# Performance work log

Hardware: AMD Instinct MI355X
Metric: run time of the kernel (lower is better)

## Reference

```python
import jax, jax.numpy as jnp
import numpy as np

EPS = 1e-5
DN = ('NCDHW', 'OIDHW', 'NCDHW')

def conv3d(x, w, b):
    y = jax.lax.conv_general_dilated(x, w, (1, 1, 1), 'SAME', dimension_numbers=DN)
    return y + b[None, :, None, None, None]

def batchnorm(x, gamma, beta):
    # training-mode BatchNorm3d: biased batch stats over (N, D, H, W) per channel
    mean = jnp.mean(x, axis=(0, 2, 3, 4), keepdims=True)
    var = jnp.mean((x - mean) ** 2, axis=(0, 2, 3, 4), keepdims=True)
    xhat = (x - mean) * jax.lax.rsqrt(var + EPS)
    return gamma[None, :, None, None, None] * xhat + beta[None, :, None, None, None]

def setup_inputs() -> dict:
    key = jax.random.key(0)
    ks = jax.random.split(key, 8)
    C, N = 32, 4  # channel, fuzzynum
    B, D, H, W = 4, 64, 64, 64
    x = jax.random.normal(ks[0], (B, C, D, H, W), dtype=jnp.float32)
    fan1 = C * 27
    conv1_w = jax.random.uniform(ks[1], (1, C, 3, 3, 3), jnp.float32, -1, 1) / np.sqrt(fan1)
    conv1_b = jnp.zeros((1,), jnp.float32)
    fan2 = 1 * 27
    conv2_w = jax.random.uniform(ks[2], (C, 1, 3, 3, 3), jnp.float32, -1, 1) / np.sqrt(fan2)
    conv2_b = jnp.zeros((C,), jnp.float32)
    mu = jax.random.normal(ks[3], (C, N), dtype=jnp.float32)
    sigma = jax.random.normal(ks[4], (C, N), dtype=jnp.float32)
    bn1_g = jnp.ones((1,), jnp.float32)
    bn1_b = jnp.zeros((1,), jnp.float32)
    bn2_g = jnp.ones((C,), jnp.float32)
    bn2_b = jnp.zeros((C,), jnp.float32)
    return {"x": x, "conv1_w": conv1_w, "conv1_b": conv1_b, "conv2_w": conv2_w,
            "conv2_b": conv2_b, "mu": mu, "sigma": sigma,
            "bn1_g": bn1_g, "bn1_b": bn1_b, "bn2_g": bn2_g, "bn2_b": bn2_b}

def reference(x, conv1_w, conv1_b, conv2_w, conv2_b, mu, sigma, bn1_g, bn1_b, bn2_g, bn2_b):
    x1 = conv3d(x, conv1_w, conv1_b)                      # [B,1,D,H,W]
    # fuzzy Gaussian membership: only channel 0 of mu/sigma is used (x1 has 1 channel)
    m = mu[0]                                             # [n]
    s = sigma[0]                                          # [n]
    z = (x1[..., None] - m) / s                           # [B,1,D,H,W,n]
    fuzz = jnp.exp(-jnp.sum(z * z, axis=-1))              # [B,1,D,H,W]
    y = batchnorm(fuzz, bn1_g, bn1_b)
    y = conv3d(y, conv2_w, conv2_b)                       # [B,C,D,H,W]
    return batchnorm(y, bn2_g, bn2_b)
```

## Files before the change

kernel.cpp:

```cpp
#include <hip/hip_runtime.h>

constexpr int Cc = 32;
constexpr int SP = 64 * 64 * 64;
constexpr int TS = 4 * SP;


__global__ __launch_bounds__(256) void k_conv1_fuzzy(
    const float* __restrict__ x, const float* __restrict__ w1,
    const float* __restrict__ b1, const float* __restrict__ mu,
    const float* __restrict__ sg, float* __restrict__ fuzz,
    float* __restrict__ acc)
{
    const int tid = threadIdx.x;
    const int t = blockIdx.x * 256 + tid;
    const int wq = t & 15;        const int w0 = wq << 2;
    const int zp = (t >> 4) & 31; const int z0 = zp << 1;
    const int y  = (t >> 9) & 63;
    const int b  = t >> 15;
    const int lane = tid & 63;

    float S1 = 0.f, S2 = 0.f, S3 = 0.f;
#pragma unroll
    for (int n = 0; n < 4; n++) {
        float m = mu[n], s = sg[n];
        float iv = 1.0f / (s * s);
        S1 += iv; S2 += m * iv; S3 += m * m * iv;
    }

    const float b1v = b1[0];
    float a00 = b1v, a01 = b1v, a02 = b1v, a03 = b1v;
    float a10 = b1v, a11 = b1v, a12 = b1v, a13 = b1v;

    const float* xb = x + (size_t)b * Cc * SP;

    for (int c = 0; c < Cc; c++) {
        const float* xc = xb + c * SP;
        const float* wc = w1 + c * 27;

        float4 M[4][3];
#pragma unroll
        for (int rz = 0; rz < 4; rz++) {
            const int zz = z0 - 1 + rz;
            const bool okz = (unsigned)zz < 64u;
#pragma unroll
            for (int dy = 0; dy < 3; dy++) {
                const int yy = y - 1 + dy;
                float4 m = make_float4(0.f, 0.f, 0.f, 0.f);
                if (okz && (unsigned)yy < 64u)
                    m = *(const float4*)(xc + (zz << 12) + (yy << 6) + w0);
                M[rz][dy] = m;
            }
        }

        float L[4][3], R[4][3];
#pragma unroll
        for (int rz = 0; rz < 4; rz++)
#pragma unroll
            for (int dy = 0; dy < 3; dy++) {
                float lv = __shfl(M[rz][dy].w, (lane + 63) & 63, 64);
                float rv = __shfl(M[rz][dy].x, (lane + 1) & 63, 64);
                L[rz][dy] = (wq > 0)  ? lv : 0.f;
                R[rz][dy] = (wq < 15) ? rv : 0.f;
            }

#pragma unroll
        for (int rz = 0; rz < 4; rz++) {
#pragma unroll
            for (int dy = 0; dy < 3; dy++) {
                const float v0 = L[rz][dy];
                const float v1 = M[rz][dy].x, v2 = M[rz][dy].y;
                const float v3 = M[rz][dy].z, v4 = M[rz][dy].w;
                const float v5 = R[rz][dy];
                if (rz < 3) {
                    const float* wr = wc + (rz * 3 + dy) * 3;
                    const float W0 = wr[0], W1 = wr[1], W2 = wr[2];
                    a00 = fmaf(v0, W0, fmaf(v1, W1, fmaf(v2, W2, a00)));
                    a01 = fmaf(v1, W0, fmaf(v2, W1, fmaf(v3, W2, a01)));
                    a02 = fmaf(v2, W0, fmaf(v3, W1, fmaf(v4, W2, a02)));
                    a03 = fmaf(v3, W0, fmaf(v4, W1, fmaf(v5, W2, a03)));
                }
                if (rz >= 1) {
                    const float* wr = wc + ((rz - 1) * 3 + dy) * 3;
                    const float W0 = wr[0], W1 = wr[1], W2 = wr[2];
                    a10 = fmaf(v0, W0, fmaf(v1, W1, fmaf(v2, W2, a10)));
                    a11 = fmaf(v1, W0, fmaf(v2, W1, fmaf(v3, W2, a11)));
                    a12 = fmaf(v2, W0, fmaf(v3, W1, fmaf(v4, W2, a12)));
                    a13 = fmaf(v3, W0, fmaf(v4, W1, fmaf(v5, W2, a13)));
                }
            }
        }
    }

    float fsum = 0.f, fsq = 0.f;
#pragma unroll
    for (int oz = 0; oz < 2; oz++) {
        float xv[4] = { oz ? a10 : a00, oz ? a11 : a01,
                        oz ? a12 : a02, oz ? a13 : a03 };
        float4 fv;
        float* fp = &fv.x;
#pragma unroll
        for (int ow = 0; ow < 4; ow++) {
            float x1 = xv[ow];
            float tt = x1 * x1 * S1 - 2.0f * x1 * S2 + S3;
            float fz = __expf(-tt);
            fp[ow] = fz;
            fsum += fz; fsq += fz * fz;
        }
        *(float4*)(fuzz + (size_t)b * SP + ((z0 + oz) << 12) + (y << 6) + w0) = fv;
    }

#pragma unroll
    for (int m = 1; m < 64; m <<= 1) {
        fsum += __shfl_xor(fsum, m, 64);
        fsq  += __shfl_xor(fsq,  m, 64);
    }
    __shared__ float red[8];
    int wid = tid >> 6;
    if ((tid & 63) == 0) { red[wid * 2] = fsum; red[wid * 2 + 1] = fsq; }
    __syncthreads();
    if (tid == 0) {
        atomicAdd(&acc[0], red[0] + red[2] + red[4] + red[6]);
        atomicAdd(&acc[1], red[1] + red[3] + red[5] + red[7]);
    }
}

__global__ void k_fin1(const float* __restrict__ g, const float* __restrict__ be,
                       float* __restrict__ acc)
{
    float mean = acc[0] * (1.0f / TS);
    float var  = acc[1] * (1.0f / TS) - mean * mean;
    float a = g[0] * rsqrtf(var + 1e-5f);
    acc[2] = a;
    acc[3] = be[0] - mean * a;
}

__global__ __launch_bounds__(256) void k_conv2(
    const float* __restrict__ fuzz, const float* __restrict__ w2,
    const float* __restrict__ b2, const float* __restrict__ acc,
    float* __restrict__ out)
{
    const int p = blockIdx.x * 256 + threadIdx.x;
    const int w = p & 63, y = (p >> 6) & 63, z = (p >> 12) & 63, b = p >> 18;
    const float a = acc[2], sh = acc[3];
    const bool wl = (w > 0), wr = (w < 63);
    const float* fb = fuzz + (size_t)b * SP;

    float v[27];
#pragma unroll
    for (int dz = 0; dz < 3; dz++) {
        int zz = z + dz - 1;
        bool mz = (unsigned)zz < 64u;
#pragma unroll
        for (int dy = 0; dy < 3; dy++) {
            int yy = y + dy - 1;
            bool my = (unsigned)yy < 64u;
            int i = (dz * 3 + dy) * 3;
            float vl = 0.f, vm = 0.f, vr = 0.f;
            if (mz && my) {
                const float* row = fb + (zz << 12) + (yy << 6) + w;
                vm = fmaf(a, row[0], sh);
                if (wl) vl = fmaf(a, row[-1], sh);
                if (wr) vr = fmaf(a, row[1], sh);
            }
            v[i] = vl; v[i + 1] = vm; v[i + 2] = vr;
        }
    }

    float* ob = out + (size_t)b * Cc * SP + (p - b * SP);
#pragma unroll 4
    for (int c = 0; c < Cc; c++) {
        const float* wc = w2 + c * 27;
        float o = b2[c];
#pragma unroll
        for (int j = 0; j < 27; j++) o = fmaf(v[j], wc[j], o);
        ob[(size_t)c * SP] = o;
    }
}

__global__ __launch_bounds__(256) void k_stats2(const float4* __restrict__ out4,
                                                float* __restrict__ acc)
{
    int blk = blockIdx.x;
    int c = (blk >> 5) & 31;
    const float4* pp = out4 + (size_t)blk * 2048 + threadIdx.x;
    float s = 0.f, q = 0.f;
#pragma unroll
    for (int i = 0; i < 8; i++) {
        float4 v = pp[i * 256];
        s += v.x + v.y + v.z + v.w;
        q += v.x * v.x + v.y * v.y + v.z * v.z + v.w * v.w;
    }
#pragma unroll
    for (int m = 1; m < 64; m <<= 1) {
        s += __shfl_xor(s, m, 64);
        q += __shfl_xor(q, m, 64);
    }
    __shared__ float red[8];
    int lane = threadIdx.x & 63, wid = threadIdx.x >> 6;
    if (lane == 0) { red[wid * 2] = s; red[wid * 2 + 1] = q; }
    __syncthreads();
    if (threadIdx.x == 0) {
        atomicAdd(&acc[4 + c],  red[0] + red[2] + red[4] + red[6]);
        atomicAdd(&acc[36 + c], red[1] + red[3] + red[5] + red[7]);
    }
}

__global__ void k_fin2(const float* __restrict__ g, const float* __restrict__ be,
                       float* __restrict__ acc)
{
    int c = threadIdx.x;
    float mean = acc[4 + c] * (1.0f / TS);
    float var  = acc[36 + c] * (1.0f / TS) - mean * mean;
    float sc = g[c] * rsqrtf(var + 1e-5f);
    acc[68 + c]  = sc;
    acc[100 + c] = be[c] - mean * sc;
}

__global__ __launch_bounds__(256) void k_norm(float4* __restrict__ out4,
                                              const float* __restrict__ acc)
{
    size_t i = (size_t)blockIdx.x * 256 + threadIdx.x;
    int c = (int)((i >> 16) & 31);
    float sc = acc[68 + c], sh = acc[100 + c];
    float4 v = out4[i];
    v.x = fmaf(v.x, sc, sh);
    v.y = fmaf(v.y, sc, sh);
    v.z = fmaf(v.z, sc, sh);
    v.w = fmaf(v.w, sc, sh);
    out4[i] = v;
}

extern "C" void kernel_launch(void* const* d_in, const int* in_sizes, int n_in,
                              void* d_out, int out_size, void* d_ws, size_t ws_size,
                              hipStream_t stream)
{
    const float* x   = (const float*)d_in[0];
    const float* w1  = (const float*)d_in[1];
    const float* b1  = (const float*)d_in[2];
    const float* w2  = (const float*)d_in[3];
    const float* b2  = (const float*)d_in[4];
    const float* mu  = (const float*)d_in[5];
    const float* sg  = (const float*)d_in[6];
    const float* g1  = (const float*)d_in[7];
    const float* be1 = (const float*)d_in[8];
    const float* g2  = (const float*)d_in[9];
    const float* be2 = (const float*)d_in[10];

    float* out  = (float*)d_out;
    float* fuzz = (float*)d_ws;
    float* acc  = fuzz + TS;

    hipMemsetAsync(acc, 0, 132 * sizeof(float), stream);
    k_conv1_fuzzy<<<512, 256, 0, stream>>>(x, w1, b1, mu, sg, fuzz, acc);
    k_fin1<<<1, 1, 0, stream>>>(g1, be1, acc);
    k_conv2<<<TS / 256, 256, 0, stream>>>(fuzz, w2, b2, acc, out);
    k_stats2<<<4096, 256, 0, stream>>>((const float4*)out, acc);
    k_fin2<<<1, 32, 0, stream>>>(g2, be2, acc);
    k_norm<<<32768, 256, 0, stream>>>((float4*)out, acc);
}
```

Measured before the change: 439.9 us.

## Recompute conv2 for stats and fuse normalization into a single output write

Conv2 is now computed twice. The first pass produces only per-channel sums and sums of squares, reduced in shared memory and never written to memory. The second pass recomputes conv2 and writes the normalized output directly. This removes one full write and two full read/write passes over the 134 MB output tensor, at the cost of doubling the cheap conv2 arithmetic and the fuzz reads. It also register-blocks several z outputs per thread, shares neighbors across lanes with wave shuffles, and double-buffers the conv1 channel loads so the next channel's loads are issued before the current channel's compute.

```diff
diff --git a/kernel.cpp b/kernel.cpp
--- a/kernel.cpp
+++ b/kernel.cpp
@@ -33,55 +33,51 @@
 
     const float* xb = x + (size_t)b * Cc * SP;
 
-    for (int c = 0; c < Cc; c++) {
-        const float* xc = xb + c * SP;
+    bool pv[12]; int ofs[12];
+#pragma unroll
+    for (int rz = 0; rz < 4; rz++) {
+        const int zz = z0 - 1 + rz;
+        const bool okz = (unsigned)zz < 64u;
+#pragma unroll
+        for (int dy = 0; dy < 3; dy++) {
+            const int yy = y - 1 + dy;
+            pv[rz * 3 + dy]  = okz && ((unsigned)yy < 64u);
+            ofs[rz * 3 + dy] = (zz << 12) + (yy << 6) + w0;
+        }
+    }
+
+    auto LOADCH = [&](int c, float4 (&M)[12]) {
+        const float* xc = xb + (size_t)c * SP;
+#pragma unroll
+        for (int i = 0; i < 12; i++)
+            M[i] = pv[i] ? *(const float4*)(xc + ofs[i])
+                         : make_float4(0.f, 0.f, 0.f, 0.f);
+    };
+
+    auto COMPUTECH = [&](int c, const float4 (&M)[12]) {
         const float* wc = w1 + c * 27;
-
-        float4 M[4][3];
+        float Wv[27];
+#pragma unroll
+        for (int k = 0; k < 27; k++) Wv[k] = wc[k];
 #pragma unroll
         for (int rz = 0; rz < 4; rz++) {
-            const int zz = z0 - 1 + rz;
-            const bool okz = (unsigned)zz < 64u;
 #pragma unroll
             for (int dy = 0; dy < 3; dy++) {
-                const int yy = y - 1 + dy;
-                float4 m = make_float4(0.f, 0.f, 0.f, 0.f);
-                if (okz && (unsigned)yy < 64u)
-                    m = *(const float4*)(xc + (zz << 12) + (yy << 6) + w0);
-                M[rz][dy] = m;
-            }
-        }
-
-        float L[4][3], R[4][3];
-#pragma unroll
-        for (int rz = 0; rz < 4; rz++)
-#pragma unroll
-            for (int dy = 0; dy < 3; dy++) {
-                float lv = __shfl(M[rz][dy].w, (lane + 63) & 63, 64);
-                float rv = __shfl(M[rz][dy].x, (lane + 1) & 63, 64);
-                L[rz][dy] = (wq > 0)  ? lv : 0.f;
-                R[rz][dy] = (wq < 15) ? rv : 0.f;
-            }
-
-#pragma unroll
-        for (int rz = 0; rz < 4; rz++) {
-#pragma unroll
-            for (int dy = 0; dy < 3; dy++) {
-                const float v0 = L[rz][dy];
-                const float v1 = M[rz][dy].x, v2 = M[rz][dy].y;
-                const float v3 = M[rz][dy].z, v4 = M[rz][dy].w;
-                const float v5 = R[rz][dy];
+                const float4 m = M[rz * 3 + dy];
+                const float lv = __shfl(m.w, (lane + 63) & 63, 64);
+                const float rv = __shfl(m.x, (lane + 1) & 63, 64);
+                const float v0 = (wq > 0)  ? lv : 0.f;
+                const float v5 = (wq < 15) ? rv : 0.f;
+                const float v1 = m.x, v2 = m.y, v3 = m.z, v4 = m.w;
                 if (rz < 3) {
-                    const float* wr = wc + (rz * 3 + dy) * 3;
-                    const float W0 = wr[0], W1 = wr[1], W2 = wr[2];
+                    const float W0 = Wv[(rz*3+dy)*3], W1 = Wv[(rz*3+dy)*3+1], W2 = Wv[(rz*3+dy)*3+2];
                     a00 = fmaf(v0, W0, fmaf(v1, W1, fmaf(v2, W2, a00)));
                     a01 = fmaf(v1, W0, fmaf(v2, W1, fmaf(v3, W2, a01)));
                     a02 = fmaf(v2, W0, fmaf(v3, W1, fmaf(v4, W2, a02)));
                     a03 = fmaf(v3, W0, fmaf(v4, W1, fmaf(v5, W2, a03)));
                 }
                 if (rz >= 1) {
-                    const float* wr = wc + ((rz - 1) * 3 + dy) * 3;
-                    const float W0 = wr[0], W1 = wr[1], W2 = wr[2];
+                    const float W0 = Wv[((rz-1)*3+dy)*3], W1 = Wv[((rz-1)*3+dy)*3+1], W2 = Wv[((rz-1)*3+dy)*3+2];
                     a10 = fmaf(v0, W0, fmaf(v1, W1, fmaf(v2, W2, a10)));
                     a11 = fmaf(v1, W0, fmaf(v2, W1, fmaf(v3, W2, a11)));
                     a12 = fmaf(v2, W0, fmaf(v3, W1, fmaf(v4, W2, a12)));
@@ -89,6 +85,15 @@
                 }
             }
         }
+    };
+
+    float4 Ma[12], Mb[12];
+    LOADCH(0, Ma);
+    for (int c = 0; c < Cc; c += 2) {
+        LOADCH(c + 1, Mb);
+        COMPUTECH(c, Ma);
+        if (c + 2 < Cc) LOADCH(c + 2, Ma);
+        COMPUTECH(c + 1, Mb);
     }
 
     float fsum = 0.f, fsq = 0.f;
@@ -96,26 +101,23 @@
     for (int oz = 0; oz < 2; oz++) {
         float xv[4] = { oz ? a10 : a00, oz ? a11 : a01,
                         oz ? a12 : a02, oz ? a13 : a03 };
-        float4 fv;
-        float* fp = &fv.x;
+        float4 fv; float* fp = &fv.x;
 #pragma unroll
         for (int ow = 0; ow < 4; ow++) {
             float x1 = xv[ow];
             float tt = x1 * x1 * S1 - 2.0f * x1 * S2 + S3;
             float fz = __expf(-tt);
-            fp[ow] = fz;
-            fsum += fz; fsq += fz * fz;
+            fp[ow] = fz; fsum += fz; fsq += fz * fz;
         }
         *(float4*)(fuzz + (size_t)b * SP + ((z0 + oz) << 12) + (y << 6) + w0) = fv;
     }
-
 #pragma unroll
     for (int m = 1; m < 64; m <<= 1) {
         fsum += __shfl_xor(fsum, m, 64);
         fsq  += __shfl_xor(fsq,  m, 64);
     }
     __shared__ float red[8];
-    int wid = tid >> 6;
+    const int wid = tid >> 6;
     if ((tid & 63) == 0) { red[wid * 2] = fsum; red[wid * 2 + 1] = fsq; }
     __syncthreads();
     if (tid == 0) {
@@ -134,74 +136,81 @@
     acc[3] = be[0] - mean * a;
 }
 
-__global__ __launch_bounds__(256) void k_conv2(
+__global__ __launch_bounds__(256) void k_conv2_stats(
     const float* __restrict__ fuzz, const float* __restrict__ w2,
-    const float* __restrict__ b2, const float* __restrict__ acc,
-    float* __restrict__ out)
-{
-    const int p = blockIdx.x * 256 + threadIdx.x;
-    const int w = p & 63, y = (p >> 6) & 63, z = (p >> 12) & 63, b = p >> 18;
+    const float* __restrict__ b2, float* __restrict__ acc)
+{
+    const int tid = threadIdx.x;
+    const int t = blockIdx.x * 256 + tid;
+    const int lane = tid & 63;
+    const int w = t & 63;
+    const int y = (t >> 6) & 63;
+    const int z0 = ((t >> 12) & 15) << 2;
+    const int b = t >> 16;
     const float a = acc[2], sh = acc[3];
-    const bool wl = (w > 0), wr = (w < 63);
     const float* fb = fuzz + (size_t)b * SP;
 
-    float v[27];
-#pragma unroll
-    for (int dz = 0; dz < 3; dz++) {
-        int zz = z + dz - 1;
-        bool mz = (unsigned)zz < 64u;
+    float Fl[6][3], Fm[6][3], Fr[6][3];
+#pragma unroll
+    for (int rz = 0; rz < 6; rz++) {
+        const int zz = z0 - 1 + rz;
+        const bool okz = (unsigned)zz < 64u;
 #pragma unroll
         for (int dy = 0; dy < 3; dy++) {
-            int yy = y + dy - 1;
-            bool my = (unsigned)yy < 64u;
-            int i = (dz * 3 + dy) * 3;
-            float vl = 0.f, vm = 0.f, vr = 0.f;
-            if (mz && my) {
-                const float* row = fb + (zz << 12) + (yy << 6) + w;
-                vm = fmaf(a, row[0], sh);
-                if (wl) vl = fmaf(a, row[-1], sh);
-                if (wr) vr = fmaf(a, row[1], sh);
-            }
-            v[i] = vl; v[i + 1] = vm; v[i + 2] = vr;
-        }
-    }
-
-    float* ob = out + (size_t)b * Cc * SP + (p - b * SP);
-#pragma unroll 4
+            const int yy = y - 1 + dy;
+            float f = 0.f;
+            if (okz && (unsigned)yy < 64u)
+                f = fmaf(a, fb[(zz << 12) + (yy << 6) + w], sh);
+            const float lv = __shfl(f, (lane + 63) & 63, 64);
+            const float rv = __shfl(f, (lane + 1) & 63, 64);
+            Fm[rz][dy] = f;
+            Fl[rz][dy] = (w > 0)  ? lv : 0.f;
+            Fr[rz][dy] = (w < 63) ? rv : 0.f;
+        }
+    }
+
+    __shared__ float red[2][32][4];
+    const int wid = tid >> 6;
+
+#pragma unroll
     for (int c = 0; c < Cc; c++) {
         const float* wc = w2 + c * 27;
-        float o = b2[c];
-#pragma unroll
-        for (int j = 0; j < 27; j++) o = fmaf(v[j], wc[j], o);
-        ob[(size_t)c * SP] = o;
-    }
-}
-
-__global__ __launch_bounds__(256) void k_stats2(const float4* __restrict__ out4,
-                                                float* __restrict__ acc)
-{
-    int blk = blockIdx.x;
-    int c = (blk >> 5) & 31;
-    const float4* pp = out4 + (size_t)blk * 2048 + threadIdx.x;
-    float s = 0.f, q = 0.f;
-#pragma unroll
-    for (int i = 0; i < 8; i++) {
-        float4 v = pp[i * 256];
-        s += v.x + v.y + v.z + v.w;
-        q += v.x * v.x + v.y * v.y + v.z * v.z + v.w * v.w;
-    }
-#pragma unroll
-    for (int m = 1; m < 64; m <<= 1) {
-        s += __shfl_xor(s, m, 64);
-        q += __shfl_xor(q, m, 64);
-    }
-    __shared__ float red[8];
-    int lane = threadIdx.x & 63, wid = threadIdx.x >> 6;
-    if (lane == 0) { red[wid * 2] = s; red[wid * 2 + 1] = q; }
+        float Wv[27];
+#pragma unroll
+        for (int k = 0; k < 27; k++) Wv[k] = wc[k];
+        const float bb = b2[c];
+        float o0 = bb, o1 = bb, o2 = bb, o3 = bb;
+#pragma unroll
+        for (int rz = 0; rz < 6; rz++) {
+#pragma unroll
+            for (int dy = 0; dy < 3; dy++) {
+                const float l = Fl[rz][dy], m = Fm[rz][dy], r = Fr[rz][dy];
+#pragma unroll
+                for (int oz = 0; oz < 4; oz++) {
+                    const int dz = rz - oz;
+                    if (dz < 0 || dz > 2) continue;
+                    const float W0 = Wv[(dz*3+dy)*3], W1 = Wv[(dz*3+dy)*3+1], W2 = Wv[(dz*3+dy)*3+2];
+                    if      (oz == 0) o0 = fmaf(l, W0, fmaf(m, W1, fmaf(r, W2, o0)));
+                    else if (oz == 1) o1 = fmaf(l, W0, fmaf(m, W1, fmaf(r, W2, o1)));
+                    else if (oz == 2) o2 = fmaf(l, W0, fmaf(m, W1, fmaf(r, W2, o2)));
+                    else              o3 = fmaf(l, W0, fmaf(m, W1, fmaf(r, W2, o3)));
+                }
+            }
+        }
+        float ps = (o0 + o1) + (o2 + o3);
+        float pq = fmaf(o0, o0, fmaf(o1, o1, fmaf(o2, o2, o3 * o3)));
+#pragma unroll
+        for (int mm = 1; mm < 64; mm <<= 1) {
+            ps += __shfl_xor(ps, mm, 64);
+            pq += __shfl_xor(pq, mm, 64);
+        }
+        if (lane == 0) { red[0][c][wid] = ps; red[1][c][wid] = pq; }
+    }
     __syncthreads();
-    if (threadIdx.x == 0) {
-        atomicAdd(&acc[4 + c],  red[0] + red[2] + red[4] + red[6]);
-        atomicAdd(&acc[36 + c], red[1] + red[3] + red[5] + red[7]);
+    if (tid < 64) {
+        const int c = tid & 31, st = tid >> 5;
+        const float v = red[st][c][0] + red[st][c][1] + red[st][c][2] + red[st][c][3];
+        atomicAdd(&acc[4 + st * 32 + c], v);
     }
 }
 
@@ -216,18 +225,68 @@
     acc[100 + c] = be[c] - mean * sc;
 }
 
-__global__ __launch_bounds__(256) void k_norm(float4* __restrict__ out4,
-                                              const float* __restrict__ acc)
-{
-    size_t i = (size_t)blockIdx.x * 256 + threadIdx.x;
-    int c = (int)((i >> 16) & 31);
-    float sc = acc[68 + c], sh = acc[100 + c];
-    float4 v = out4[i];
-    v.x = fmaf(v.x, sc, sh);
-    v.y = fmaf(v.y, sc, sh);
-    v.z = fmaf(v.z, sc, sh);
-    v.w = fmaf(v.w, sc, sh);
-    out4[i] = v;
+__global__ __launch_bounds__(256) void k_conv2_write(
+    const float* __restrict__ fuzz, const float* __restrict__ w2,
+    const float* __restrict__ b2, const float* __restrict__ acc,
+    float* __restrict__ out)
+{
+    const int tid = threadIdx.x;
+    const int t = blockIdx.x * 256 + tid;
+    const int lane = tid & 63;
+    const int w = t & 63;
+    const int y = (t >> 6) & 63;
+    const int z0 = ((t >> 12) & 31) << 1;
+    const int b = t >> 17;
+    const float a = acc[2], sh = acc[3];
+    const float* fb = fuzz + (size_t)b * SP;
+
+    float Fl[4][3], Fm[4][3], Fr[4][3];
+#pragma unroll
+    for (int rz = 0; rz < 4; rz++) {
+        const int zz = z0 - 1 + rz;
+        const bool okz = (unsigned)zz < 64u;
+#pragma unroll
+        for (int dy = 0; dy < 3; dy++) {
+            const int yy = y - 1 + dy;
+            float f = 0.f;
+            if (okz && (unsigned)yy < 64u)
+                f = fmaf(a, fb[(zz << 12) + (yy << 6) + w], sh);
+            const float lv = __shfl(f, (lane + 63) & 63, 64);
+            const float rv = __shfl(f, (lane + 1) & 63, 64);
+            Fm[rz][dy] = f;
+            Fl[rz][dy] = (w > 0)  ? lv : 0.f;
+            Fr[rz][dy] = (w < 63) ? rv : 0.f;
+        }
+    }
+
+    float* ob = out + (size_t)b * Cc * SP + (z0 << 12) + (y << 6) + w;
+#pragma unroll
+    for (int c = 0; c < Cc; c++) {
+        const float* wc = w2 + c * 27;
+        float Wv[27];
+#pragma unroll
+        for (int k = 0; k < 27; k++) Wv[k] = wc[k];
+        const float bb = b2[c];
+        float o0 = bb, o1 = bb;
+#pragma unroll
+        for (int rz = 0; rz < 4; rz++) {
+#pragma unroll
+            for (int dy = 0; dy < 3; dy++) {
+                const float l = Fl[rz][dy], m = Fm[rz][dy], r = Fr[rz][dy];
+#pragma unroll
+                for (int oz = 0; oz < 2; oz++) {
+                    const int dz = rz - oz;
+                    if (dz < 0 || dz > 2) continue;
+                    const float W0 = Wv[(dz*3+dy)*3], W1 = Wv[(dz*3+dy)*3+1], W2 = Wv[(dz*3+dy)*3+2];
+                    if (oz == 0) o0 = fmaf(l, W0, fmaf(m, W1, fmaf(r, W2, o0)));
+                    else         o1 = fmaf(l, W0, fmaf(m, W1, fmaf(r, W2, o1)));
+                }
+            }
+        }
+        const float sc = acc[68 + c], shf = acc[100 + c];
+        ob[(size_t)c * SP]        = fmaf(o0, sc, shf);
+        ob[(size_t)c * SP + 4096] = fmaf(o1, sc, shf);
+    }
 }
 
 extern "C" void kernel_launch(void* const* d_in, const int* in_sizes, int n_in,
@@ -253,8 +312,7 @@
     hipMemsetAsync(acc, 0, 132 * sizeof(float), stream);
     k_conv1_fuzzy<<<512, 256, 0, stream>>>(x, w1, b1, mu, sg, fuzz, acc);
     k_fin1<<<1, 1, 0, stream>>>(g1, be1, acc);
-    k_conv2<<<TS / 256, 256, 0, stream>>>(fuzz, w2, b2, acc, out);
-    k_stats2<<<4096, 256, 0, stream>>>((const float4*)out, acc);
+    k_conv2_stats<<<1024, 256, 0, stream>>>(fuzz, w2, b2, acc);
     k_fin2<<<1, 32, 0, stream>>>(g2, be2, acc);
-    k_norm<<<32768, 256, 0, stream>>>((float4*)out, acc);
-}
+    k_conv2_write<<<2048, 256, 0, stream>>>(fuzz, w2, b2, acc, out);
+}
```

Measured after the change: 414.1 us. 1.06x faster.
